# Kernel tuning notes

Hardware: AMD Instinct MI355X
Metric: run time of the kernel (lower is better)

Reference implementation:

```python
import jax, jax.numpy as jnp
import numpy as np

N_NODES = 50000
N_EDGES = 800000
N_FEAT = 512
N_HID = 256
N_LAYER = 4
N_CLASS = 40


def setup_inputs() -> dict:
    key = jax.random.key(0)
    ks = jax.random.split(key, 16)
    x = jax.random.normal(ks[0], (N_NODES, N_FEAT), dtype=jnp.float32)
    edge_index = jax.random.randint(ks[1], (2, N_EDGES), 0, N_NODES, dtype=jnp.int64 if jax.config.jax_enable_x64 else jnp.int32)

    def glorot(k, fan_in, fan_out):
        lim = np.sqrt(6.0 / (fan_in + fan_out)).astype(np.float32)
        return jax.random.uniform(k, (fan_in, fan_out), jnp.float32, -lim, lim)

    in_gc_W = glorot(ks[2], N_FEAT, N_HID)
    in_gc_b = jnp.zeros((N_HID,), jnp.float32)
    in_lin_W = glorot(ks[3], N_FEAT, N_HID)
    in_lin_b = jnp.zeros((N_HID,), jnp.float32)
    # n_layer-1 = 3 hidden conv / lin pairs, stacked on leading axis
    convs_W = jnp.stack([glorot(jax.random.fold_in(ks[4], i), N_HID, N_HID) for i in range(N_LAYER - 1)])
    convs_b = jnp.zeros((N_LAYER - 1, N_HID), jnp.float32)
    lins_W = jnp.stack([glorot(jax.random.fold_in(ks[5], i), N_HID, N_HID) for i in range(N_LAYER - 1)])
    lins_b = jnp.zeros((N_LAYER - 1, N_HID), jnp.float32)
    out_W = glorot(ks[6], N_HID * N_LAYER, N_CLASS)
    out_b = jnp.zeros((N_CLASS,), jnp.float32)
    return {
        "x": x, "edge_index": edge_index,
        "in_gc_W": in_gc_W, "in_gc_b": in_gc_b,
        "in_lin_W": in_lin_W, "in_lin_b": in_lin_b,
        "convs_W": convs_W, "convs_b": convs_b,
        "lins_W": lins_W, "lins_b": lins_b,
        "out_W": out_W, "out_b": out_b,
    }


def reference(x, edge_index, in_gc_W, in_gc_b, in_lin_W, in_lin_b,
              convs_W, convs_b, lins_W, lins_b, out_W, out_b):
    src, dst = edge_index[0], edge_index[1]
    n = x.shape[0]
    # GCN symmetric normalization with self-loops: deg = 1 + in-degree
    deg = jnp.zeros((n,), jnp.float32).at[dst].add(1.0) + 1.0
    dinv = jax.lax.rsqrt(deg)
    edge_norm = dinv[src] * dinv[dst]        # [E]
    self_norm = dinv * dinv                  # [N]

    def gcn(h, W, b):
        hw = h @ W                           # [N, out]
        msg = hw[src] * edge_norm[:, None]   # gather + scale
        agg = jax.ops.segment_sum(msg, dst, num_segments=n)
        agg = agg + hw * self_norm[:, None]  # self-loop term
        return agg + b

    # inductive: GCNConv + linear residual; dropout = identity (eval mode)
    h = jax.nn.relu(gcn(x, in_gc_W, in_gc_b) + x @ in_lin_W + in_lin_b)
    xs = [h]
    for i in range(convs_W.shape[0]):
        h = jax.nn.relu(gcn(h, convs_W[i], convs_b[i]) + h @ lins_W[i] + lins_b[i])
        xs.append(h)
    # JumpingKnowledge mode='cat'
    jk = jnp.concatenate(xs, axis=-1)        # [N, n_hid * n_layer]
    return jk @ out_W + out_b
```

## Files before the change

kernel.cpp:

```cpp
#include <hip/hip_runtime.h>

typedef _Float16 half8 __attribute__((ext_vector_type(8)));
typedef _Float16 half4 __attribute__((ext_vector_type(4)));
typedef float floatx4 __attribute__((ext_vector_type(4)));

__device__ __forceinline__ void gld16(const _Float16* g, _Float16* lds_base) {
    __builtin_amdgcn_global_load_lds(
        (const __attribute__((address_space(1))) unsigned int*)g,
        (__attribute__((address_space(3))) unsigned int*)lds_base,
        16, 0, 0);
}

__global__ __launch_bounds__(256) void zero_i32(int* __restrict__ p, int n) {
    int i = blockIdx.x * 256 + threadIdx.x;
    if (i < n) p[i] = 0;
}

__global__ __launch_bounds__(256) void hist_dst(const int* __restrict__ dst,
                                                int* __restrict__ count, int E) {
    int e = blockIdx.x * 256 + threadIdx.x;
    if (e < E) atomicAdd(&count[dst[e]], 1);
}

__global__ __launch_bounds__(256) void cast_f32_f16(const float* __restrict__ in,
                                                    _Float16* __restrict__ out, int n4) {
    int i = blockIdx.x * 256 + threadIdx.x;
    if (i < n4) {
        float4 v = *(const float4*)&in[(size_t)i * 4];
        half4 h = { (_Float16)v.x, (_Float16)v.y, (_Float16)v.z, (_Float16)v.w };
        *(half4*)&out[(size_t)i * 4] = h;
    }
}

__global__ __launch_bounds__(256) void transpose_cast_tiled(
    const float* __restrict__ W, _Float16* __restrict__ WT, int K, int N)
{
    __shared__ _Float16 t[32][33];
    const int k0 = blockIdx.x * 32, n0 = blockIdx.y * 32;
    const int tx = threadIdx.x & 31, ty = threadIdx.x >> 5;
    #pragma unroll
    for (int i = 0; i < 4; ++i) {
        int k = k0 + ty + i * 8, n = n0 + tx;
        float v = (k < K && n < N) ? W[(size_t)k * N + n] : 0.0f;
        t[ty + i * 8][tx] = (_Float16)v;
    }
    __syncthreads();
    #pragma unroll
    for (int i = 0; i < 4; ++i) {
        int n = n0 + ty + i * 8, k = k0 + tx;
        if (n < N && k < K) WT[(size_t)n * K + k] = t[tx][ty + i * 8];
    }
}

__global__ __launch_bounds__(256) void scan_block(const int* __restrict__ count,
                                                  int* __restrict__ incl,
                                                  int* __restrict__ blocksum,
                                                  float* __restrict__ dinv, int n) {
    __shared__ int tmp[256];
    int t = threadIdx.x;
    int i = blockIdx.x * 256 + t;
    int v = (i < n) ? count[i] : 0;
    if (i < n) dinv[i] = rsqrtf(1.0f + (float)v);
    tmp[t] = v;
    __syncthreads();
    for (int off = 1; off < 256; off <<= 1) {
        int x = (t >= off) ? tmp[t - off] : 0;
        __syncthreads();
        tmp[t] += x;
        __syncthreads();
    }
    if (i < n) incl[i] = tmp[t];
    if (t == 255) blocksum[blockIdx.x] = tmp[255];
}

__global__ __launch_bounds__(256) void scan_top(const int* __restrict__ blocksum,
                                                int* __restrict__ blockoff, int nb) {
    __shared__ int tmp[256];
    int t = threadIdx.x;
    int v = (t < nb) ? blocksum[t] : 0;
    tmp[t] = v;
    __syncthreads();
    for (int off = 1; off < 256; off <<= 1) {
        int x = (t >= off) ? tmp[t - off] : 0;
        __syncthreads();
        tmp[t] += x;
        __syncthreads();
    }
    if (t < nb) blockoff[t] = tmp[t] - v;
}

__global__ __launch_bounds__(256) void make_rowptr(const int* __restrict__ incl,
                                                   const int* __restrict__ count,
                                                   const int* __restrict__ blockoff,
                                                   int* __restrict__ rowptr,
                                                   int* __restrict__ cursor, int n) {
    int i = blockIdx.x * 256 + threadIdx.x;
    if (i < n) {
        int r = incl[i] - count[i] + blockoff[blockIdx.x];
        rowptr[i] = r;
        cursor[i] = r;
    }
}

__global__ __launch_bounds__(256) void scatter_perm(const int* __restrict__ src,
                                                    const int* __restrict__ dst,
                                                    const float* __restrict__ dinv,
                                                    int* __restrict__ cursor,
                                                    int2* __restrict__ sorted_meta, int E) {
    int e = blockIdx.x * 256 + threadIdx.x;
    if (e < E) {
        int d = dst[e], s = src[e];
        int slot = atomicAdd(&cursor[d], 1);
        sorted_meta[slot] = make_int2(s, __float_as_int(dinv[s] * dinv[d]));
    }
}

template<bool DUAL>
__global__ __launch_bounds__(256) void gemm_mfma(
    const _Float16* __restrict__ A, int lda,
    const _Float16* __restrict__ BT, int Nrows,
    const float* __restrict__ bias0, const float* __restrict__ bias1,
    _Float16* __restrict__ lin_h, _Float16* __restrict__ hw,
    float* __restrict__ Cf, int ldc,
    int M, int K)
{
    __shared__ _Float16 As[128 * 64];
    __shared__ _Float16 Bs[128 * 64];

    const int tid  = threadIdx.x;
    const int wave = tid >> 6;
    const int lane = tid & 63;
    const int q    = lane >> 4;
    const int r    = lane & 15;

    const int wm = (wave & 1) * 64;
    const int wn = (wave >> 1) * 64;

    const int bn = blockIdx.x * 128;
    const int bm = blockIdx.y * 128;

    const int srow  = wave * 32;
    const int lrow8 = lane >> 3;
    const int cp    = lane & 7;

    floatx4 acc[4][4] = {};

    for (int k0 = 0; k0 < K; k0 += 64) {
        #pragma unroll
        for (int t = 0; t < 4; ++t) {
            int lrow = srow + t * 8 + lrow8;
            int c    = cp ^ (lrow & 7);
            int gm = bm + lrow; if (gm > M - 1) gm = M - 1;
            gld16(&A[(size_t)gm * lda + k0 + c * 8], &As[(srow + t * 8) * 64]);
            int gn = bn + lrow; if (gn > Nrows - 1) gn = Nrows - 1;
            gld16(&BT[(size_t)gn * K + k0 + c * 8], &Bs[(srow + t * 8) * 64]);
        }
        __syncthreads();

        #pragma unroll
        for (int kk = 0; kk < 2; ++kk) {
            const int sc = ((kk << 2) | q) ^ (r & 7);
            half8 af[4], bf[4];
            #pragma unroll
            for (int mi = 0; mi < 4; ++mi)
                af[mi] = *(const half8*)&As[(wm + mi * 16 + r) * 64 + sc * 8];
            #pragma unroll
            for (int ni = 0; ni < 4; ++ni)
                bf[ni] = *(const half8*)&Bs[(wn + ni * 16 + r) * 64 + sc * 8];
            #pragma unroll
            for (int mi = 0; mi < 4; ++mi)
                #pragma unroll
                for (int ni = 0; ni < 4; ++ni)
                    acc[mi][ni] = __builtin_amdgcn_mfma_f32_16x16x32_f16(
                        af[mi], bf[ni], acc[mi][ni], 0, 0, 0);
        }
        __syncthreads();
    }

    if (DUAL) {
        const bool islin = (bn < 256);
        _Float16* dstp = islin ? lin_h : hw;
        #pragma unroll
        for (int ni = 0; ni < 4; ++ni) {
            int col = bn + wn + ni * 16 + r;
            int c2  = islin ? col : col - 256;
            float badd = islin ? (bias0[col] + bias1[col]) : 0.0f;
            #pragma unroll
            for (int mi = 0; mi < 4; ++mi)
                #pragma unroll
                for (int reg = 0; reg < 4; ++reg) {
                    int gm = bm + wm + mi * 16 + q * 4 + reg;
                    if (gm < M)
                        dstp[(size_t)gm * 256 + c2] = (_Float16)(acc[mi][ni][reg] + badd);
                }
        }
    } else {
        #pragma unroll
        for (int ni = 0; ni < 4; ++ni) {
            int col = bn + wn + ni * 16 + r;
            if (col >= Nrows) continue;
            float badd = bias0 ? bias0[col] : 0.0f;
            #pragma unroll
            for (int mi = 0; mi < 4; ++mi)
                #pragma unroll
                for (int reg = 0; reg < 4; ++reg) {
                    int gm = bm + wm + mi * 16 + q * 4 + reg;
                    if (gm < M)
                        Cf[(size_t)gm * ldc + col] = acc[mi][ni][reg] + badd;
                }
        }
    }
}

__global__ __launch_bounds__(256) void aggregate_csr(
    const int* __restrict__ rowptr, const int* __restrict__ count,
    const int2* __restrict__ sorted_meta,
    const float* __restrict__ dinv,
    const _Float16* __restrict__ hw,
    const _Float16* __restrict__ lin_h,
    _Float16* __restrict__ jk_col, int n)
{
    int wave = (blockIdx.x * 256 + threadIdx.x) >> 6;
    int lane = threadIdx.x & 63;
    if (wave >= n) return;
    const int i = wave;
    const int h  = lane >> 5;
    const int fl = lane & 31;

    const int start = rowptr[i];
    const int deg   = count[i];

    float accf[8];
    if (h == 0) {
        half8 l8 = *(const half8*)&lin_h[(size_t)i * 256 + fl * 8];
        #pragma unroll
        for (int t = 0; t < 8; ++t) accf[t] = (float)l8[t];
    } else {
        float di = dinv[i];
        float sn = di * di;
        half8 s8 = *(const half8*)&hw[(size_t)i * 256 + fl * 8];
        #pragma unroll
        for (int t = 0; t < 8; ++t) accf[t] = (float)s8[t] * sn;
    }

    for (int base = 0; base < deg; base += 64) {
        int m = deg - base;
        if (m > 64) m = 64;
        int2 meta = make_int2(0, 0);
        if (lane < m) meta = sorted_meta[start + base + lane];

        for (int j = 0; j < m; j += 8) {
            half8 hv[4];
            float nm[4];
            #pragma unroll
            for (int k2 = 0; k2 < 4; ++k2) {
                int e   = j + k2 * 2 + h;
                int idx = (e < m) ? e : (m - 1);
                int s   = __shfl(meta.x, idx, 64);
                int nmb = __shfl(meta.y, idx, 64);
                nm[k2]  = (e < m) ? __int_as_float(nmb) : 0.0f;
                hv[k2]  = *(const half8*)&hw[(size_t)s * 256 + fl * 8];
            }
            #pragma unroll
            for (int k2 = 0; k2 < 4; ++k2)
                #pragma unroll
                for (int t = 0; t < 8; ++t)
                    accf[t] = fmaf((float)hv[k2][t], nm[k2], accf[t]);
        }
    }

    #pragma unroll
    for (int t = 0; t < 8; ++t)
        accf[t] += __shfl_xor(accf[t], 32, 64);

    if (h == 0) {
        half8 o;
        #pragma unroll
        for (int t = 0; t < 8; ++t) o[t] = (_Float16)fmaxf(accf[t], 0.0f);
        *(half8*)&jk_col[(size_t)i * 1024 + fl * 8] = o;
    }
}

extern "C" void kernel_launch(void* const* d_in, const int* in_sizes, int n_in,
                              void* d_out, int out_size, void* d_ws, size_t ws_size,
                              hipStream_t stream) {
    const float* x        = (const float*)d_in[0];
    const int*   ei       = (const int*)d_in[1];
    const float* in_gc_W  = (const float*)d_in[2];
    const float* in_gc_b  = (const float*)d_in[3];
    const float* in_lin_W = (const float*)d_in[4];
    const float* in_lin_b = (const float*)d_in[5];
    const float* convs_W  = (const float*)d_in[6];
    const float* convs_b  = (const float*)d_in[7];
    const float* lins_W   = (const float*)d_in[8];
    const float* lins_b   = (const float*)d_in[9];
    const float* out_W    = (const float*)d_in[10];
    const float* out_b    = (const float*)d_in[11];

    const int N = 50000;
    const int E = in_sizes[1] / 2;
    const int F = 512, H = 256, L = 4, NC = 40;

    const int* src = ei;
    const int* dst = ei + E;

    char* ws = (char*)d_ws;
    auto carve = [&](size_t bytes) { void* p = ws; ws += (bytes + 255) & ~(size_t)255; return p; };
    float*    dinv        = (float*)carve((size_t)N * 4);
    int*      count       = (int*)  carve((size_t)N * 4);
    int*      incl        = (int*)  carve((size_t)N * 4);
    int*      rowptr      = (int*)  carve((size_t)N * 4);
    int*      cursor      = (int*)  carve((size_t)N * 4);
    int*      blocksum    = (int*)  carve(256 * 4);
    int*      blockoff    = (int*)  carve(256 * 4);
    int2*     sorted_meta = (int2*) carve((size_t)E * 8);
    _Float16* xh          = (_Float16*)carve((size_t)N * F * 2);
    _Float16* w0comb      = (_Float16*)carve((size_t)512 * F * 2);
    _Float16* wcomb       = (_Float16*)carve((size_t)3 * 512 * H * 2);
    _Float16* outWT       = (_Float16*)carve((size_t)NC * H * L * 2);
    _Float16* lin_h       = (_Float16*)carve((size_t)N * H * 2);
    _Float16* hw          = (_Float16*)carve((size_t)N * H * 2);
    _Float16* jk_h        = (_Float16*)carve((size_t)N * H * L * 2);
    float*    out         = (float*)d_out;

    const int nbN = (N + 255) / 256;
    const int nbE = (E + 255) / 256;

    zero_i32<<<nbN, 256, 0, stream>>>(count, N);
    hist_dst<<<nbE, 256, 0, stream>>>(dst, count, E);
    scan_block<<<nbN, 256, 0, stream>>>(count, incl, blocksum, dinv, N);
    scan_top<<<1, 256, 0, stream>>>(blocksum, blockoff, nbN);
    make_rowptr<<<nbN, 256, 0, stream>>>(incl, count, blockoff, rowptr, cursor, N);
    scatter_perm<<<nbE, 256, 0, stream>>>(src, dst, dinv, cursor, sorted_meta, E);

    cast_f32_f16<<<(N * F / 4 + 255) / 256, 256, 0, stream>>>(x, xh, N * F / 4);
    {
        dim3 tg((F + 31) / 32, (H + 31) / 32);
        transpose_cast_tiled<<<tg, 256, 0, stream>>>(in_lin_W, w0comb,                F, H);
        transpose_cast_tiled<<<tg, 256, 0, stream>>>(in_gc_W,  w0comb + (size_t)H * F, F, H);
        dim3 th((H + 31) / 32, (H + 31) / 32);
        for (int l = 0; l < 3; ++l) {
            _Float16* wl = wcomb + (size_t)l * 512 * H;
            transpose_cast_tiled<<<th, 256, 0, stream>>>(lins_W  + (size_t)l * H * H, wl,                 H, H);
            transpose_cast_tiled<<<th, 256, 0, stream>>>(convs_W + (size_t)l * H * H, wl + (size_t)H * H, H, H);
        }
        dim3 to((H * L + 31) / 32, (NC + 31) / 32);
        transpose_cast_tiled<<<to, 256, 0, stream>>>(out_W, outWT, H * L, NC);
    }

    const dim3 dgrid(4, (N + 127) / 128);
    const dim3 ogrid(1, (N + 127) / 128);
    const int agg_blocks = (N + 3) / 4;

    for (int l = 0; l < L; ++l) {
        const _Float16* Ah = (l == 0) ? xh : (jk_h + (size_t)(l - 1) * H);
        int lda            = (l == 0) ? F : H * L;
        int K              = (l == 0) ? F : H;
        const _Float16* BT = (l == 0) ? w0comb : (wcomb + (size_t)(l - 1) * 512 * H);
        const float* gcB   = (l == 0) ? in_gc_b  : (convs_b + (size_t)(l - 1) * H);
        const float* liB   = (l == 0) ? in_lin_b : (lins_b  + (size_t)(l - 1) * H);

        gemm_mfma<true><<<dgrid, 256, 0, stream>>>(Ah, lda, BT, 512, liB, gcB,
                                                   lin_h, hw, nullptr, 0, N, K);
        aggregate_csr<<<agg_blocks, 256, 0, stream>>>(rowptr, count, sorted_meta,
                                                      dinv, hw, lin_h, jk_h + (size_t)l * H, N);
    }

    gemm_mfma<false><<<ogrid, 256, 0, stream>>>(jk_h, H * L, outWT, NC, out_b, nullptr,
                                                nullptr, nullptr, out, NC, N, H * L);
}
```

Baseline: 740.9 us.

## Split CSR aggregation across feature halves with four edge groups per wave

Each node's aggregation is now split across two blocks, each handling half of the 256 features, and the launch doubles the block count to match. Inside a wave, four 16-lane groups gather four edges at once instead of two 32-lane groups gathering two. Partial sums are combined with two cross-lane shuffle reductions. The aim is more waves and more independent gathers in flight, to hide latency in the memory-bound sparse gather. The cost is that edge metadata and row pointers are read twice, once per feature half, and each gather segment is narrower.

```diff
diff --git a/kernel.cpp b/kernel.cpp
--- a/kernel.cpp
+++ b/kernel.cpp
@@ -220,25 +220,31 @@
     const _Float16* __restrict__ lin_h,
     _Float16* __restrict__ jk_col, int n)
 {
-    int wave = (blockIdx.x * 256 + threadIdx.x) >> 6;
-    int lane = threadIdx.x & 63;
-    if (wave >= n) return;
-    const int i = wave;
-    const int h  = lane >> 5;
-    const int fl = lane & 31;
+    const int bx    = blockIdx.x;
+    const int xslot = bx & 7;
+    const int half  = xslot >> 2;
+    const int chunk = ((bx >> 3) << 2) + (xslot & 3);
+    const int wave  = threadIdx.x >> 6;
+    const int lane  = threadIdx.x & 63;
+    const int i     = chunk * 4 + wave;
+    if (i >= n) return;
+
+    const int qw = lane >> 4;
+    const int fl = lane & 15;
+    const int fbase = half * 128 + fl * 8;
 
     const int start = rowptr[i];
     const int deg   = count[i];
 
-    float accf[8];
-    if (h == 0) {
-        half8 l8 = *(const half8*)&lin_h[(size_t)i * 256 + fl * 8];
+    float accf[8] = {};
+    if (qw == 0) {
+        half8 l8 = *(const half8*)&lin_h[(size_t)i * 256 + fbase];
         #pragma unroll
         for (int t = 0; t < 8; ++t) accf[t] = (float)l8[t];
-    } else {
+    } else if (qw == 1) {
         float di = dinv[i];
         float sn = di * di;
-        half8 s8 = *(const half8*)&hw[(size_t)i * 256 + fl * 8];
+        half8 s8 = *(const half8*)&hw[(size_t)i * 256 + fbase];
         #pragma unroll
         for (int t = 0; t < 8; ++t) accf[t] = (float)s8[t] * sn;
     }
@@ -249,17 +255,17 @@
         int2 meta = make_int2(0, 0);
         if (lane < m) meta = sorted_meta[start + base + lane];
 
-        for (int j = 0; j < m; j += 8) {
+        for (int j = 0; j < m; j += 16) {
             half8 hv[4];
             float nm[4];
             #pragma unroll
             for (int k2 = 0; k2 < 4; ++k2) {
-                int e   = j + k2 * 2 + h;
+                int e   = j + k2 * 4 + qw;
                 int idx = (e < m) ? e : (m - 1);
                 int s   = __shfl(meta.x, idx, 64);
                 int nmb = __shfl(meta.y, idx, 64);
                 nm[k2]  = (e < m) ? __int_as_float(nmb) : 0.0f;
-                hv[k2]  = *(const half8*)&hw[(size_t)s * 256 + fl * 8];
+                hv[k2]  = *(const half8*)&hw[(size_t)s * 256 + fbase];
             }
             #pragma unroll
             for (int k2 = 0; k2 < 4; ++k2)
@@ -270,14 +276,16 @@
     }
 
     #pragma unroll
-    for (int t = 0; t < 8; ++t)
+    for (int t = 0; t < 8; ++t) {
+        accf[t] += __shfl_xor(accf[t], 16, 64);
         accf[t] += __shfl_xor(accf[t], 32, 64);
-
-    if (h == 0) {
+    }
+
+    if (qw == 0) {
         half8 o;
         #pragma unroll
         for (int t = 0; t < 8; ++t) o[t] = (_Float16)fmaxf(accf[t], 0.0f);
-        *(half8*)&jk_col[(size_t)i * 1024 + fl * 8] = o;
+        *(half8*)&jk_col[(size_t)i * 1024 + fbase] = o;
     }
 }
 
@@ -350,7 +358,7 @@
 
     const dim3 dgrid(4, (N + 127) / 128);
     const dim3 ogrid(1, (N + 127) / 128);
-    const int agg_blocks = (N + 3) / 4;
+    const int agg_blocks = 2 * ((N + 3) / 4);
 
     for (int l = 0; l < L; ++l) {
         const _Float16* Ah = (l == 0) ? xh : (jk_h + (size_t)(l - 1) * H);
```

Result: faster. 725.8 us (-2.0%).
